# Performance work log

Measured on AMD Instinct MI355X. Metric: run time of the kernel, lower is better.

## Reference

```python
import jax, jax.numpy as jnp
import numpy as np

B, S, H = 8, 512, 768
NH, DH = 12, 64
I = 3072
E = 8
TOPK = 2
EPS = 1e-12


def _ln(x, g, b):
    m = jnp.mean(x, axis=-1, keepdims=True)
    v = jnp.mean(jnp.square(x - m), axis=-1, keepdims=True)
    return (x - m) * jax.lax.rsqrt(v + EPS) * g + b


def setup_inputs() -> dict:
    key = jax.random.key(0)
    ks = jax.random.split(key, 20)
    s_h = 1.0 / np.sqrt(H)
    s_i = 1.0 / np.sqrt(I)
    inp = {
        "hidden_states": jax.random.normal(ks[0], (B, S, H), jnp.float32),
        "Wq": jax.random.normal(ks[1], (H, H), jnp.float32) * s_h,
        "bq": jnp.zeros((H,), jnp.float32),
        "Wk": jax.random.normal(ks[2], (H, H), jnp.float32) * s_h,
        "bk": jnp.zeros((H,), jnp.float32),
        "Wv": jax.random.normal(ks[3], (H, H), jnp.float32) * s_h,
        "bv": jnp.zeros((H,), jnp.float32),
        "Wo": jax.random.normal(ks[4], (H, H), jnp.float32) * s_h,
        "bo": jnp.zeros((H,), jnp.float32),
        "ln_attn_g": jnp.ones((H,), jnp.float32),
        "ln_attn_b": jnp.zeros((H,), jnp.float32),
        "ln_ffn_g": jnp.ones((H,), jnp.float32),
        "ln_ffn_b": jnp.zeros((H,), jnp.float32),
        "Wr": jax.random.normal(ks[5], (H, E), jnp.float32) * s_h,
        "br": jnp.zeros((E,), jnp.float32),
        "W_up": jax.random.normal(ks[6], (E, H, I), jnp.float32) * s_h,
        "b_up": jnp.zeros((E, I), jnp.float32),
        "W_new": jax.random.normal(ks[7], (E, H, I), jnp.float32) * s_h,
        "b_new": jnp.zeros((E, I), jnp.float32),
        "W_down": jax.random.normal(ks[8], (E, I, H), jnp.float32) * s_i,
        "b_down": jnp.zeros((E, H), jnp.float32),
    }
    return inp


def reference(hidden_states, Wq, bq, Wk, bk, Wv, bv, Wo, bo,
              ln_attn_g, ln_attn_b, ln_ffn_g, ln_ffn_b,
              Wr, br, W_up, b_up, W_new, b_new, W_down, b_down):
    x = hidden_states
    # --- BertSelfAttention ---
    q = (x @ Wq + bq).reshape(B, S, NH, DH).transpose(0, 2, 1, 3)
    k = (x @ Wk + bk).reshape(B, S, NH, DH).transpose(0, 2, 1, 3)
    v = (x @ Wv + bv).reshape(B, S, NH, DH).transpose(0, 2, 1, 3)
    scores = jnp.einsum("bhqd,bhkd->bhqk", q, k) / np.sqrt(DH)
    probs = jax.nn.softmax(scores, axis=-1)
    ctx = jnp.einsum("bhqk,bhkd->bhqd", probs, v)
    ctx = ctx.transpose(0, 2, 1, 3).reshape(B, S, H)
    # --- BertSelfOutput: dense + residual + LayerNorm ---
    attention_output = _ln(ctx @ Wo + bo + x, ln_attn_g, ln_attn_b)
    # --- feed_forward_chunk: LayerNorm then token top-k MoE ---
    xl = _ln(attention_output, ln_ffn_g, ln_ffn_b)
    router_logits = xl @ Wr + br                      # [B,S,E]
    router_probs = jax.nn.softmax(router_logits, axis=-1)
    topw, topi = jax.lax.top_k(router_probs, TOPK)    # [B,S,K]
    topw = topw / jnp.sum(topw, axis=-1, keepdims=True)
    gates = jnp.sum(jax.nn.one_hot(topi, E, dtype=xl.dtype) * topw[..., None], axis=-2)  # [B,S,E]
    # --- experts (BertExpert: gelu(up(x)) * new(x) -> down), dense over E ---
    up = jax.nn.gelu(jnp.einsum("bsh,ehi->ebsi", xl, W_up) + b_up[:, None, None, :], approximate=False)
    gate_h = jnp.einsum("bsh,ehi->ebsi", xl, W_new) + b_new[:, None, None, :]
    y = jnp.einsum("ebsi,eih->ebsh", up * gate_h, W_down) + b_down[:, None, None, :]
    moe_out = jnp.einsum("ebsh,bse->bsh", y, gates)
    layer_output = moe_out + attention_output
    return layer_output, router_logits
```

## Files before the change

kernel.cpp:

```cpp
#include <hip/hip_runtime.h>
#include <hip/hip_bf16.h>
#include <cmath>


constexpr int cB = 8, cS = 512, cH = 768, cNH = 12, cDH = 64, cI = 3072, cE = 8;
constexpr int cT = cB * cS;
constexpr size_t TH = (size_t)cT * cH;

typedef __hip_bfloat16 bf16;
typedef __attribute__((ext_vector_type(8))) short s8v;
typedef __attribute__((ext_vector_type(4))) float f4v;

constexpr size_t SZ_WEXP     = (size_t)cE * cI * cH / 2;
constexpr size_t OFF_WUP_T   = 0;
constexpr size_t OFF_WNEW_T  = OFF_WUP_T + SZ_WEXP;
constexpr size_t OFF_WDOWN_T = OFF_WNEW_T + SZ_WEXP;
constexpr size_t OFF_QKV     = OFF_WDOWN_T + SZ_WEXP;
constexpr size_t OFF_CTX     = OFF_QKV + 4 * TH;
constexpr size_t OFF_XLB     = OFF_CTX + TH;
constexpr size_t OFF_WGT     = OFF_XLB + TH / 2;
constexpr size_t OFF_COUNTS  = OFF_WGT + 2 * cT;
constexpr size_t OFF_LISTS   = OFF_COUNTS + 16;

__device__ __forceinline__ void glds16(const void* g, void* l) {
    __builtin_amdgcn_global_load_lds(
        (const __attribute__((address_space(1))) unsigned int*)g,
        (__attribute__((address_space(3))) unsigned int*)l, 16, 0, 0);
}

__global__ void init_counts_kernel(int* __restrict__ counts) {
    if (threadIdx.x < cE) counts[threadIdx.x] = 0;
}

__global__ __launch_bounds__(256) void transpose_bf16_kernel(
    const float* __restrict__ src, bf16* __restrict__ dst, int R, int C) {
    __shared__ float tile[64][65];
    const size_t zb = (size_t)blockIdx.z * R * C;
    const int r0 = blockIdx.y * 64, c0 = blockIdx.x * 64;
    const int t = threadIdx.x;
    const int lr = t >> 4, lc = (t & 15) * 4;
#pragma unroll
    for (int i = 0; i < 4; ++i) {
        float4 v = *(const float4*)(src + zb + (size_t)(r0 + lr + i * 16) * C + c0 + lc);
        tile[lr + i * 16][lc + 0] = v.x; tile[lr + i * 16][lc + 1] = v.y;
        tile[lr + i * 16][lc + 2] = v.z; tile[lr + i * 16][lc + 3] = v.w;
    }
    __syncthreads();
#pragma unroll
    for (int i = 0; i < 4; ++i) {
        int cr = lr + i * 16;
        bf16 o[4];
#pragma unroll
        for (int j = 0; j < 4; ++j) o[j] = (bf16)tile[lc + j][cr];
        *(uint2*)(dst + zb + (size_t)(c0 + cr) * R + r0 + lc) = *(uint2*)o;
    }
}

__device__ __forceinline__ void gemm_body128(
    const float* __restrict__ A, const float* __restrict__ B,
    const float* __restrict__ bias, float* __restrict__ C,
    int N, int K, int m0, int n0, int kbeg, int kend, bool addb) {
    __shared__ float As[16 * 132];
    __shared__ float Bs[16 * 128];
    const int t = threadIdx.x;
    const int tx = t & 15, ty = t >> 4;
    const int ar = t >> 2, ac = (t & 3) * 4;
    const float* gB0 = B + (size_t)(kbeg + (t >> 5)) * N + n0 + (t & 31) * 4;
    float* dB0 = Bs + t * 4;
    const float* gA0 = A + (size_t)(m0 + ar) * K + kbeg + ac;
    const float* gA1 = A + (size_t)(m0 + ar + 64) * K + kbeg + ac;
    float acc[8][8] = {};
    float4 a0 = *(const float4*)gA0;
    float4 a1 = *(const float4*)gA1;
    for (int k0 = kbeg; k0 < kend; k0 += 16) {
        glds16(gB0, dB0);
        glds16(gB0 + (size_t)8 * N, dB0 + 1024);
        As[(ac + 0) * 132 + ar] = a0.x; As[(ac + 1) * 132 + ar] = a0.y;
        As[(ac + 2) * 132 + ar] = a0.z; As[(ac + 3) * 132 + ar] = a0.w;
        As[(ac + 0) * 132 + ar + 64] = a1.x; As[(ac + 1) * 132 + ar + 64] = a1.y;
        As[(ac + 2) * 132 + ar + 64] = a1.z; As[(ac + 3) * 132 + ar + 64] = a1.w;
        __syncthreads();
        if (k0 + 16 < kend) {
            gA0 += 16; gA1 += 16;
            a0 = *(const float4*)gA0;
            a1 = *(const float4*)gA1;
        }
#pragma unroll
        for (int kk = 0; kk < 16; ++kk) {
            float a[8], b[8];
            *(float4*)&a[0] = *(const float4*)&As[kk * 132 + ty * 8];
            *(float4*)&a[4] = *(const float4*)&As[kk * 132 + ty * 8 + 4];
            *(float4*)&b[0] = *(const float4*)&Bs[kk * 128 + tx * 4];
            *(float4*)&b[4] = *(const float4*)&Bs[kk * 128 + tx * 4 + 64];
#pragma unroll
            for (int i = 0; i < 8; ++i)
#pragma unroll
                for (int j = 0; j < 8; ++j) acc[i][j] += a[i] * b[j];
        }
        __syncthreads();
        gB0 += (size_t)16 * N;
    }
#pragma unroll
    for (int i = 0; i < 8; ++i) {
        int m = m0 + ty * 8 + i;
        float4 o0, o1;
        o0.x = acc[i][0]; o0.y = acc[i][1]; o0.z = acc[i][2]; o0.w = acc[i][3];
        o1.x = acc[i][4]; o1.y = acc[i][5]; o1.z = acc[i][6]; o1.w = acc[i][7];
        if (addb) {
            o0.x += bias[n0 + tx * 4 + 0]; o0.y += bias[n0 + tx * 4 + 1];
            o0.z += bias[n0 + tx * 4 + 2]; o0.w += bias[n0 + tx * 4 + 3];
            o1.x += bias[n0 + 64 + tx * 4 + 0]; o1.y += bias[n0 + 64 + tx * 4 + 1];
            o1.z += bias[n0 + 64 + tx * 4 + 2]; o1.w += bias[n0 + 64 + tx * 4 + 3];
        }
        *(float4*)(C + (size_t)m * N + n0 + tx * 4) = o0;
        *(float4*)(C + (size_t)m * N + n0 + 64 + tx * 4) = o1;
    }
}

__global__ __launch_bounds__(256) void gemm_qkv_kernel(
    const float* __restrict__ A,
    const float* __restrict__ Wq, const float* __restrict__ Wk,
    const float* __restrict__ Wv,
    const float* __restrict__ bq, const float* __restrict__ bk,
    const float* __restrict__ bv,
    float* __restrict__ q0, float* __restrict__ k0, float* __restrict__ v0,
    float* __restrict__ q1, float* __restrict__ k1, float* __restrict__ v1) {
    const int f = blockIdx.x + 6 * blockIdx.y + 192 * blockIdx.z;
    const int xcd = f & 7, p = f >> 3;
    const int yl = p & 3;
    const int n  = (p >> 2) % 6;
    const int pz = p / 24;
    const int y  = xcd * 4 + yl;
    const int proj = pz >> 1, ks = pz & 1;
    const float* B = (proj == 0) ? Wq : (proj == 1) ? Wk : Wv;
    const float* bias = (proj == 0) ? bq : (proj == 1) ? bk : bv;
    float* C = (proj == 0) ? (ks ? q1 : q0)
             : (proj == 1) ? (ks ? k1 : k0)
                           : (ks ? v1 : v0);
    gemm_body128(A, B, bias, C, cH, cH, y * 128, n * 128,
                 ks * 384, ks * 384 + 384, ks == 0);
}

__global__ __launch_bounds__(256) void reduce_qkv_kernel(
    float* __restrict__ dst2, const float* __restrict__ src2,
    float* __restrict__ v0, const float* __restrict__ v1) {
    const size_t n2 = 2 * TH / 4, n3 = 3 * TH / 4;
    for (size_t i = (size_t)blockIdx.x * 256 + threadIdx.x; i < n3;
         i += (size_t)gridDim.x * 256) {
        if (i < n2) {
            float4 a = ((const float4*)dst2)[i];
            float4 b = ((const float4*)src2)[i];
            a.x += b.x; a.y += b.y; a.z += b.z; a.w += b.w;
            ((float4*)dst2)[i] = a;
        } else {
            size_t j = i - n2;
            float4 a = ((const float4*)v0)[j];
            float4 b = ((const float4*)v1)[j];
            a.x += b.x; a.y += b.y; a.z += b.z; a.w += b.w;
            ((float4*)v0)[j] = a;
        }
    }
}

__global__ __launch_bounds__(256) void gemm_wo_kernel(
    const float* __restrict__ A, const float* __restrict__ W,
    const float* __restrict__ bias,
    float* __restrict__ p0, float* __restrict__ p1,
    float* __restrict__ p2, float* __restrict__ p3) {
    const int f = blockIdx.x + 6 * blockIdx.y + 192 * blockIdx.z;
    const int xcd = f & 7, p = f >> 3;
    const int yl = p & 3;
    const int n  = (p >> 2) % 6;
    const int ks = p / 24;
    const int y  = xcd * 4 + yl;
    float* C = (ks == 0) ? p0 : (ks == 1) ? p1 : (ks == 2) ? p2 : p3;
    gemm_body128(A, W, bias, C, cH, cH, y * 128, n * 128,
                 ks * 192, ks * 192 + 192, ks == 0);
}

__global__ __launch_bounds__(256) void attn_kernel(
    const float* __restrict__ q, const float* __restrict__ k,
    const float* __restrict__ v, float* __restrict__ ctx) {
    __shared__ float sQ[64][68];
    __shared__ float sKV[64][68];
    __shared__ float sS[64][68];
    __shared__ float sM[64], sL[64], sAl[64];
    const int f = blockIdx.x + 8 * blockIdx.y + 96 * blockIdx.z;
    const int xcd = f & 7, p = f >> 3;
    const int q0 = (p & 7) * 64;
    const int hbg = xcd * 12 + (p >> 3);
    const int h = hbg % 12, b = hbg / 12;
    const int t = threadIdx.x;
    const int lr = t >> 2, lq = (t & 3) * 16;
    {
        const float* gq = q + (size_t)(b * cS + q0 + lr) * cH + h * cDH + lq;
#pragma unroll
        for (int j = 0; j < 4; ++j) {
            float4 x = *(const float4*)(gq + j * 4);
            x.x *= 0.125f; x.y *= 0.125f; x.z *= 0.125f; x.w *= 0.125f;
            *(float4*)&sQ[lr][lq + j * 4] = x;
        }
    }
    if (t < 64) { sM[t] = -1e30f; sL[t] = 0.f; }
    const int c0 = t & 15, rr = (t >> 4) * 4;
    const int d4 = (t & 15) * 4, rp = (t >> 4) * 4;
    const int sr = t >> 2, sc = (t & 3) * 16;
    float4 o_acc[4];
#pragma unroll
    for (int i = 0; i < 4; ++i) o_acc[i] = make_float4(0.f, 0.f, 0.f, 0.f);

    for (int kt = 0; kt < 8; ++kt) {
        float4 kreg[4];
        {
            const float* gk = k + (size_t)(b * cS + kt * 64 + lr) * cH + h * cDH + lq;
#pragma unroll
            for (int j = 0; j < 4; ++j) kreg[j] = *(const float4*)(gk + j * 4);
        }
        __syncthreads();
#pragma unroll
        for (int j = 0; j < 4; ++j) *(float4*)&sKV[lr][lq + j * 4] = kreg[j];
        __syncthreads();
        float accS[4][4] = {};
#pragma unroll
        for (int d = 0; d < 64; d += 4) {
            float4 qv[4], kv[4];
#pragma unroll
            for (int i = 0; i < 4; ++i) qv[i] = *(const float4*)&sQ[rr + i][d];
#pragma unroll
            for (int j = 0; j < 4; ++j) kv[j] = *(const float4*)&sKV[c0 + 16 * j][d];
#pragma unroll
            for (int i = 0; i < 4; ++i)
#pragma unroll
                for (int j = 0; j < 4; ++j)
                    accS[i][j] += qv[i].x * kv[j].x + qv[i].y * kv[j].y +
                                  qv[i].z * kv[j].z + qv[i].w * kv[j].w;
        }
#pragma unroll
        for (int i = 0; i < 4; ++i)
#pragma unroll
            for (int j = 0; j < 4; ++j) sS[rr + i][c0 + 16 * j] = accS[i][j];
        float4 vreg[4];
        {
            const float* gv = v + (size_t)(b * cS + kt * 64 + lr) * cH + h * cDH + lq;
#pragma unroll
            for (int j = 0; j < 4; ++j) vreg[j] = *(const float4*)(gv + j * 4);
        }
        __syncthreads();
        {
            float4 s[4];
#pragma unroll
            for (int j = 0; j < 4; ++j) s[j] = *(const float4*)&sS[sr][sc + j * 4];
            float m = -1e30f;
#pragma unroll
            for (int j = 0; j < 4; ++j)
                m = fmaxf(m, fmaxf(fmaxf(s[j].x, s[j].y), fmaxf(s[j].z, s[j].w)));
            m = fmaxf(m, __shfl_xor(m, 1));
            m = fmaxf(m, __shfl_xor(m, 2));
            float m_old = sM[sr];
            float m_new = fmaxf(m_old, m);
            float sum = 0.f;
#pragma unroll
            for (int j = 0; j < 4; ++j) {
                s[j].x = __expf(s[j].x - m_new); s[j].y = __expf(s[j].y - m_new);
                s[j].z = __expf(s[j].z - m_new); s[j].w = __expf(s[j].w - m_new);
                sum += s[j].x + s[j].y + s[j].z + s[j].w;
                *(float4*)&sS[sr][sc + j * 4] = s[j];
            }
            sum += __shfl_xor(sum, 1);
            sum += __shfl_xor(sum, 2);
            if ((t & 3) == 0) {
                float alpha = __expf(m_old - m_new);
                sAl[sr] = alpha;
                sM[sr] = m_new;
                sL[sr] = sL[sr] * alpha + sum;
            }
        }
#pragma unroll
        for (int j = 0; j < 4; ++j) *(float4*)&sKV[lr][lq + j * 4] = vreg[j];
        __syncthreads();
#pragma unroll
        for (int i = 0; i < 4; ++i) {
            float al = sAl[rp + i];
            o_acc[i].x *= al; o_acc[i].y *= al; o_acc[i].z *= al; o_acc[i].w *= al;
        }
        for (int kk4 = 0; kk4 < 64; kk4 += 4) {
            float4 pv[4], vv[4];
#pragma unroll
            for (int i = 0; i < 4; ++i) pv[i] = *(const float4*)&sS[rp + i][kk4];
#pragma unroll
            for (int j = 0; j < 4; ++j) vv[j] = *(const float4*)&sKV[kk4 + j][d4];
#pragma unroll
            for (int i = 0; i < 4; ++i) {
                o_acc[i].x += pv[i].x * vv[0].x + pv[i].y * vv[1].x +
                              pv[i].z * vv[2].x + pv[i].w * vv[3].x;
                o_acc[i].y += pv[i].x * vv[0].y + pv[i].y * vv[1].y +
                              pv[i].z * vv[2].y + pv[i].w * vv[3].y;
                o_acc[i].z += pv[i].x * vv[0].z + pv[i].y * vv[1].z +
                              pv[i].z * vv[2].z + pv[i].w * vv[3].z;
                o_acc[i].w += pv[i].x * vv[0].w + pv[i].y * vv[1].w +
                              pv[i].z * vv[2].w + pv[i].w * vv[3].w;
            }
        }
    }
    __syncthreads();
#pragma unroll
    for (int i = 0; i < 4; ++i) {
        float inv = 1.0f / sL[rp + i];
        float4 o = o_acc[i];
        o.x *= inv; o.y *= inv; o.z *= inv; o.w *= inv;
        *(float4*)(ctx + (size_t)(b * cS + q0 + rp + i) * cH + h * cDH + d4) = o;
    }
}

__device__ __forceinline__ float block_reduce_sum(float v, float* red) {
#pragma unroll
    for (int o = 32; o; o >>= 1) v += __shfl_xor(v, o);
    __syncthreads();
    if ((threadIdx.x & 63) == 0) red[threadIdx.x >> 6] = v;
    __syncthreads();
    return red[0] + red[1] + red[2] + red[3];
}

__global__ __launch_bounds__(256) void ln_router_kernel(
    const float* __restrict__ dense0, const float* __restrict__ dense1,
    const float* __restrict__ dense2, const float* __restrict__ dense3,
    const float* __restrict__ resid,
    const float* __restrict__ g1, const float* __restrict__ b1,
    const float* __restrict__ g2, const float* __restrict__ b2,
    const float* __restrict__ Wr, const float* __restrict__ br,
    float* __restrict__ out, bf16* __restrict__ xlb,
    float* __restrict__ out_logits, float* __restrict__ wgt,
    int* __restrict__ counts, int* __restrict__ lists) {
    __shared__ float red[4];
    __shared__ float lred[4][8];
    const int t = blockIdx.x, tid = threadIdx.x;
    const size_t base = (size_t)t * cH;
    float v[3], s = 0.f;
#pragma unroll
    for (int i = 0; i < 3; ++i) {
        size_t ix = base + tid + 256 * i;
        v[i] = dense0[ix] + dense1[ix] + dense2[ix] + dense3[ix] + resid[ix];
        s += v[i];
    }
    const float mean = block_reduce_sum(s, red) * (1.0f / cH);
    float vs = 0.f;
#pragma unroll
    for (int i = 0; i < 3; ++i) { float d = v[i] - mean; vs += d * d; }
    const float rstd = rsqrtf(block_reduce_sum(vs, red) * (1.0f / cH) + 1e-12f);
    float a[3], s2 = 0.f;
#pragma unroll
    for (int i = 0; i < 3; ++i) {
        a[i] = (v[i] - mean) * rstd * g1[tid + 256 * i] + b1[tid + 256 * i];
        out[base + tid + 256 * i] = a[i];
        s2 += a[i];
    }
    const float mean2 = block_reduce_sum(s2, red) * (1.0f / cH);
    float vs2 = 0.f;
#pragma unroll
    for (int i = 0; i < 3; ++i) { float d = a[i] - mean2; vs2 += d * d; }
    const float rstd2 = rsqrtf(block_reduce_sum(vs2, red) * (1.0f / cH) + 1e-12f);
    float xl[3];
#pragma unroll
    for (int i = 0; i < 3; ++i) {
        xl[i] = (a[i] - mean2) * rstd2 * g2[tid + 256 * i] + b2[tid + 256 * i];
        xlb[base + tid + 256 * i] = (bf16)xl[i];
    }
    float lg[cE] = {};
#pragma unroll
    for (int i = 0; i < 3; ++i) {
        const float* wr = Wr + (size_t)(tid + 256 * i) * cE;
#pragma unroll
        for (int e = 0; e < cE; ++e) lg[e] += xl[i] * wr[e];
    }
#pragma unroll
    for (int e = 0; e < cE; ++e)
#pragma unroll
        for (int o = 32; o; o >>= 1) lg[e] += __shfl_xor(lg[e], o);
    if ((tid & 63) == 0)
#pragma unroll
        for (int e = 0; e < cE; ++e) lred[tid >> 6][e] = lg[e];
    __syncthreads();
    if (tid == 0) {
        float logits[cE];
#pragma unroll
        for (int e = 0; e < cE; ++e) {
            logits[e] = lred[0][e] + lred[1][e] + lred[2][e] + lred[3][e] + br[e];
            out_logits[(size_t)t * cE + e] = logits[e];
        }
        int i0 = 0;
        for (int e = 1; e < cE; ++e) if (logits[e] > logits[i0]) i0 = e;
        int i1 = (i0 == 0) ? 1 : 0;
        for (int e = 0; e < cE; ++e)
            if (e != i0 && logits[e] > logits[i1]) i1 = e;
        float e1 = __expf(logits[i1] - logits[i0]);
        float w0 = 1.0f / (1.0f + e1);
        float w1 = e1 * w0;
        wgt[t * 2 + 0] = w0;
        wgt[t * 2 + 1] = w1;
        int p0 = atomicAdd(&counts[i0], 1);
        lists[i0 * cT + p0] = t * 2 + 0;
        int p1 = atomicAdd(&counts[i1], 1);
        lists[i1 * cT + p1] = t * 2 + 1;
    }
}

__global__ __launch_bounds__(256) void expert_up_mfma_kernel(
    const bf16* __restrict__ xlb,
    const bf16* __restrict__ WupT, const bf16* __restrict__ WnewT,
    const float* __restrict__ b_up, const float* __restrict__ b_new,
    const int* __restrict__ counts, const int* __restrict__ lists,
    bf16* __restrict__ act) {
    const int e = blockIdx.z;
    const int cnt = counts[e];
    const int m0 = blockIdx.y * 128;
    if (m0 >= cnt) return;
    const int n0 = blockIdx.x * 64;
    __shared__ short sA[128 * 32], sB1[64 * 32], sB2[64 * 32];
    __shared__ int rowa[128];
    const int t = threadIdx.x;
    if (t < 128) {
        int idx = m0 + t;
        rowa[t] = (idx < cnt) ? lists[e * cT + idx] : -1;
    }
    __syncthreads();
    const int lane = t & 63, w = t >> 6;
    const int wm = (w >> 1) * 64, wn = (w & 1) * 32;
    const int rA0 = t >> 2, kc8 = (t & 3) * 8;
    int a0 = rowa[rA0], a1 = rowa[rA0 + 64];
    const bf16* gA0 = xlb + (size_t)(a0 < 0 ? 0 : (a0 >> 1)) * cH + kc8;
    const bf16* gA1 = xlb + (size_t)(a1 < 0 ? 0 : (a1 >> 1)) * cH + kc8;
    const bf16* B1 = WupT + (size_t)e * cI * cH;
    const bf16* B2 = WnewT + (size_t)e * cI * cH;
    const bf16* gB1 = B1 + (size_t)(n0 + rA0) * cH + kc8;
    const bf16* gB2 = B2 + (size_t)(n0 + rA0) * cH + kc8;
    short* dA0 = sA + t * 8;   short* dA1 = sA + (t + 256) * 8;
    short* dB1 = sB1 + t * 8;  short* dB2 = sB2 + t * 8;
    f4v zero = {0.f, 0.f, 0.f, 0.f};
    f4v acc1[4][2], acc2[4][2];
#pragma unroll
    for (int i = 0; i < 4; ++i)
#pragma unroll
        for (int j = 0; j < 2; ++j) { acc1[i][j] = zero; acc2[i][j] = zero; }
    const int fr = lane & 15, kg = (lane >> 4) * 8;
    for (int kk = 0; kk < cH; kk += 32) {
        glds16(gA0, dA0); glds16(gA1, dA1);
        glds16(gB1, dB1); glds16(gB2, dB2);
        __syncthreads();
        s8v af[4], bf1[2], bf2[2];
#pragma unroll
        for (int i = 0; i < 4; ++i)
            af[i] = *(const s8v*)(sA + (wm + i * 16 + fr) * 32 + kg);
#pragma unroll
        for (int j = 0; j < 2; ++j) {
            bf1[j] = *(const s8v*)(sB1 + (wn + j * 16 + fr) * 32 + kg);
            bf2[j] = *(const s8v*)(sB2 + (wn + j * 16 + fr) * 32 + kg);
        }
#pragma unroll
        for (int mi = 0; mi < 4; ++mi)
#pragma unroll
            for (int ni = 0; ni < 2; ++ni) {
                acc1[mi][ni] = __builtin_amdgcn_mfma_f32_16x16x32_bf16(
                    af[mi], bf1[ni], acc1[mi][ni], 0, 0, 0);
                acc2[mi][ni] = __builtin_amdgcn_mfma_f32_16x16x32_bf16(
                    af[mi], bf2[ni], acc2[mi][ni], 0, 0, 0);
            }
        __syncthreads();
        gA0 += 32; gA1 += 32; gB1 += 32; gB2 += 32;
    }
    const int cn = lane & 15, rq = (lane >> 4) * 4;
#pragma unroll
    for (int mi = 0; mi < 4; ++mi)
#pragma unroll
        for (int r = 0; r < 4; ++r) {
            int ml = wm + mi * 16 + rq + r;
            int a = rowa[ml];
            if (a < 0) continue;
            bf16* orow = act + (size_t)a * cI + n0 + wn;
#pragma unroll
            for (int ni = 0; ni < 2; ++ni) {
                int nl = ni * 16 + cn;
                float up = acc1[mi][ni][r] + b_up[e * cI + n0 + wn + nl];
                float nw = acc2[mi][ni][r] + b_new[e * cI + n0 + wn + nl];
                float g = 0.5f * up * (1.0f + erff(up * 0.70710678118654752f));
                orow[nl] = (bf16)(g * nw);
            }
        }
}

__global__ __launch_bounds__(256) void expert_down_mfma_kernel(
    const bf16* __restrict__ act, const bf16* __restrict__ WdownT,
    const float* __restrict__ b_down,
    const int* __restrict__ counts, const int* __restrict__ lists,
    const float* __restrict__ wgt, float* __restrict__ out) {
    const int e = blockIdx.z;
    const int cnt = counts[e];
    const int m0 = blockIdx.y * 128;
    if (m0 >= cnt) return;
    const int n0 = blockIdx.x * 128;
    __shared__ short sA[128 * 32], sB[128 * 32];
    __shared__ int rowa[128];
    const int t = threadIdx.x;
    if (t < 128) {
        int idx = m0 + t;
        rowa[t] = (idx < cnt) ? lists[e * cT + idx] : -1;
    }
    __syncthreads();
    const int lane = t & 63, w = t >> 6;
    const int wm = (w >> 1) * 64, wn = (w & 1) * 64;
    const int rA0 = t >> 2, kc8 = (t & 3) * 8;
    int a0 = rowa[rA0], a1 = rowa[rA0 + 64];
    const bf16* gA0 = act + (size_t)(a0 < 0 ? 0 : a0) * cI + kc8;
    const bf16* gA1 = act + (size_t)(a1 < 0 ? 0 : a1) * cI + kc8;
    const bf16* BT = WdownT + (size_t)e * cH * cI;
    const bf16* gB0 = BT + (size_t)(n0 + rA0) * cI + kc8;
    const bf16* gB1 = BT + (size_t)(n0 + rA0 + 64) * cI + kc8;
    short* dA0 = sA + t * 8;       short* dA1 = sA + (t + 256) * 8;
    short* dB0 = sB + t * 8;       short* dB1 = sB + (t + 256) * 8;
    f4v zero = {0.f, 0.f, 0.f, 0.f};
    f4v acc[4][4];
#pragma unroll
    for (int i = 0; i < 4; ++i)
#pragma unroll
        for (int j = 0; j < 4; ++j) acc[i][j] = zero;
    const int fr = lane & 15, kg = (lane >> 4) * 8;
    for (int kk = 0; kk < cI; kk += 32) {
        glds16(gA0, dA0); glds16(gA1, dA1);
        glds16(gB0, dB0); glds16(gB1, dB1);
        __syncthreads();
        s8v af[4], bf[4];
#pragma unroll
        for (int i = 0; i < 4; ++i) af[i] = *(const s8v*)(sA + (wm + i * 16 + fr) * 32 + kg);
#pragma unroll
        for (int i = 0; i < 4; ++i) bf[i] = *(const s8v*)(sB + (wn + i * 16 + fr) * 32 + kg);
#pragma unroll
        for (int mi = 0; mi < 4; ++mi)
#pragma unroll
            for (int ni = 0; ni < 4; ++ni)
                acc[mi][ni] = __builtin_amdgcn_mfma_f32_16x16x32_bf16(
                    af[mi], bf[ni], acc[mi][ni], 0, 0, 0);
        __syncthreads();
        gA0 += 32; gA1 += 32; gB0 += 32; gB1 += 32;
    }
    const int cn = lane & 15, rq = (lane >> 4) * 4;
#pragma unroll
    for (int mi = 0; mi < 4; ++mi)
#pragma unroll
        for (int r = 0; r < 4; ++r) {
            int ml = wm + mi * 16 + rq + r;
            int a = rowa[ml];
            if (a < 0) continue;
            int token = a >> 1;
            float wv = wgt[a];
#pragma unroll
            for (int ni = 0; ni < 4; ++ni) {
                int n = n0 + wn + ni * 16 + cn;
                atomicAdd(&out[(size_t)token * cH + n],
                          wv * (acc[mi][ni][r] + b_down[e * cH + n]));
            }
        }
}

extern "C" void kernel_launch(void* const* d_in, const int* in_sizes, int n_in,
                              void* d_out, int out_size, void* d_ws, size_t ws_size,
                              hipStream_t stream) {
    const float* x      = (const float*)d_in[0];
    const float* Wq     = (const float*)d_in[1];
    const float* bq     = (const float*)d_in[2];
    const float* Wk     = (const float*)d_in[3];
    const float* bk     = (const float*)d_in[4];
    const float* Wv     = (const float*)d_in[5];
    const float* bv     = (const float*)d_in[6];
    const float* Wo     = (const float*)d_in[7];
    const float* bo     = (const float*)d_in[8];
    const float* ln1g   = (const float*)d_in[9];
    const float* ln1b   = (const float*)d_in[10];
    const float* ln2g   = (const float*)d_in[11];
    const float* ln2b   = (const float*)d_in[12];
    const float* Wr     = (const float*)d_in[13];
    const float* br     = (const float*)d_in[14];
    const float* W_up   = (const float*)d_in[15];
    const float* b_up   = (const float*)d_in[16];
    const float* W_new  = (const float*)d_in[17];
    const float* b_new  = (const float*)d_in[18];
    const float* W_down = (const float*)d_in[19];
    const float* b_down = (const float*)d_in[20];

    float* out = (float*)d_out;
    float* ws  = (float*)d_ws;

    bf16* WupT   = (bf16*)(ws + OFF_WUP_T);
    bf16* WnewT  = (bf16*)(ws + OFF_WNEW_T);
    bf16* WdownT = (bf16*)(ws + OFF_WDOWN_T);
    float* q     = ws + OFF_QKV;
    float* k     = ws + OFF_QKV + TH;
    float* v     = ws + OFF_QKV + 2 * TH;
    float* tmp   = ws + OFF_QKV + 3 * TH;
    bf16* act    = (bf16*)(ws + OFF_QKV);
    float* ctx   = ws + OFF_CTX;
    bf16* xlb    = (bf16*)(ws + OFF_XLB);
    float* wgt   = ws + OFF_WGT;
    int* counts  = (int*)(ws + OFF_COUNTS);
    int* lists   = (int*)(ws + OFF_LISTS);

    init_counts_kernel<<<1, 64, 0, stream>>>(counts);

    transpose_bf16_kernel<<<dim3(48, 12, cE), 256, 0, stream>>>(W_up, WupT, cH, cI);
    transpose_bf16_kernel<<<dim3(48, 12, cE), 256, 0, stream>>>(W_new, WnewT, cH, cI);
    transpose_bf16_kernel<<<dim3(12, 48, cE), 256, 0, stream>>>(W_down, WdownT, cI, cH);

    gemm_qkv_kernel<<<dim3(cH / 128, cT / 128, 6), 256, 0, stream>>>(
        x, Wq, Wk, Wv, bq, bk, bv, q, k, v, tmp, ctx, out);
    reduce_qkv_kernel<<<2048, 256, 0, stream>>>(q, tmp, v, out);
    attn_kernel<<<dim3(cS / 64, cNH, cB), 256, 0, stream>>>(q, k, v, ctx);
    gemm_wo_kernel<<<dim3(cH / 128, cT / 128, 4), 256, 0, stream>>>(
        ctx, Wo, bo, q, k, v, tmp);
    ln_router_kernel<<<cT, 256, 0, stream>>>(
        q, k, v, tmp, x, ln1g, ln1b, ln2g, ln2b, Wr, br,
        out, xlb, out + TH, wgt, counts, lists);

    expert_up_mfma_kernel<<<dim3(cI / 64, cT / 128, cE), 256, 0, stream>>>(
        xlb, WupT, WnewT, b_up, b_new, counts, lists, act);
    expert_down_mfma_kernel<<<dim3(cH / 128, cT / 128, cE), 256, 0, stream>>>(
        act, WdownT, b_down, counts, lists, wgt, out);
}
```

Baseline: 1.056 ms.

## Remap expert GEMM blocks so each XCD reuses one weight column tile

The expert up and down kernels now compute a linear block id and remap it so that all M-blocks sharing one (expert, N-tile) weight slice land on the same XCD, since consecutive blocks are dispatched round-robin across the eight XCDs. This is meant to improve L2 reuse of the bf16 weight tiles. The fp32 GEMM body also drops its register prefetch of the next A tile and loads A at the top of each iteration, which shortens register live ranges but exposes global load latency before the barrier. The remap relies on the grid dimensions matching the hardcoded constants.

```diff
diff --git a/kernel.cpp b/kernel.cpp
--- a/kernel.cpp
+++ b/kernel.cpp
@@ -67,12 +67,10 @@
     const int ar = t >> 2, ac = (t & 3) * 4;
     const float* gB0 = B + (size_t)(kbeg + (t >> 5)) * N + n0 + (t & 31) * 4;
     float* dB0 = Bs + t * 4;
-    const float* gA0 = A + (size_t)(m0 + ar) * K + kbeg + ac;
-    const float* gA1 = A + (size_t)(m0 + ar + 64) * K + kbeg + ac;
     float acc[8][8] = {};
-    float4 a0 = *(const float4*)gA0;
-    float4 a1 = *(const float4*)gA1;
     for (int k0 = kbeg; k0 < kend; k0 += 16) {
+        float4 a0 = *(const float4*)(A + (size_t)(m0 + ar) * K + k0 + ac);
+        float4 a1 = *(const float4*)(A + (size_t)(m0 + ar + 64) * K + k0 + ac);
         glds16(gB0, dB0);
         glds16(gB0 + (size_t)8 * N, dB0 + 1024);
         As[(ac + 0) * 132 + ar] = a0.x; As[(ac + 1) * 132 + ar] = a0.y;
@@ -80,11 +78,6 @@
         As[(ac + 0) * 132 + ar + 64] = a1.x; As[(ac + 1) * 132 + ar + 64] = a1.y;
         As[(ac + 2) * 132 + ar + 64] = a1.z; As[(ac + 3) * 132 + ar + 64] = a1.w;
         __syncthreads();
-        if (k0 + 16 < kend) {
-            gA0 += 16; gA1 += 16;
-            a0 = *(const float4*)gA0;
-            a1 = *(const float4*)gA1;
-        }
 #pragma unroll
         for (int kk = 0; kk < 16; ++kk) {
             float a[8], b[8];
@@ -410,11 +403,17 @@
     const float* __restrict__ b_up, const float* __restrict__ b_new,
     const int* __restrict__ counts, const int* __restrict__ lists,
     bf16* __restrict__ act) {
-    const int e = blockIdx.z;
+    const int hh = blockIdx.x + 48 * blockIdx.y + 1536 * blockIdx.z;
+    const int xcd = hh & 7;
+    const int r = hh >> 3;
+    const int mb = r & 31;
+    const int cq = r >> 5;
+    const int c = cq * 8 + xcd;
+    const int e = c / 48, n0b = c % 48;
     const int cnt = counts[e];
-    const int m0 = blockIdx.y * 128;
+    const int m0 = mb * 128;
     if (m0 >= cnt) return;
-    const int n0 = blockIdx.x * 64;
+    const int n0 = n0b * 64;
     __shared__ short sA[128 * 32], sB1[64 * 32], sB2[64 * 32];
     __shared__ int rowa[128];
     const int t = threadIdx.x;
@@ -471,16 +470,16 @@
 #pragma unroll
     for (int mi = 0; mi < 4; ++mi)
 #pragma unroll
-        for (int r = 0; r < 4; ++r) {
-            int ml = wm + mi * 16 + rq + r;
+        for (int r2 = 0; r2 < 4; ++r2) {
+            int ml = wm + mi * 16 + rq + r2;
             int a = rowa[ml];
             if (a < 0) continue;
             bf16* orow = act + (size_t)a * cI + n0 + wn;
 #pragma unroll
             for (int ni = 0; ni < 2; ++ni) {
                 int nl = ni * 16 + cn;
-                float up = acc1[mi][ni][r] + b_up[e * cI + n0 + wn + nl];
-                float nw = acc2[mi][ni][r] + b_new[e * cI + n0 + wn + nl];
+                float up = acc1[mi][ni][r2] + b_up[e * cI + n0 + wn + nl];
+                float nw = acc2[mi][ni][r2] + b_new[e * cI + n0 + wn + nl];
                 float g = 0.5f * up * (1.0f + erff(up * 0.70710678118654752f));
                 orow[nl] = (bf16)(g * nw);
             }
@@ -492,11 +491,17 @@
     const float* __restrict__ b_down,
     const int* __restrict__ counts, const int* __restrict__ lists,
     const float* __restrict__ wgt, float* __restrict__ out) {
-    const int e = blockIdx.z;
+    const int hh = blockIdx.x + 6 * blockIdx.y + 192 * blockIdx.z;
+    const int xcd = hh & 7;
+    const int r = hh >> 3;
+    const int mb = r & 31;
+    const int cq = r >> 5;
+    const int c = cq * 8 + xcd;
+    const int e = c / 6, n0b = c % 6;
     const int cnt = counts[e];
-    const int m0 = blockIdx.y * 128;
+    const int m0 = mb * 128;
     if (m0 >= cnt) return;
-    const int n0 = blockIdx.x * 128;
+    const int n0 = n0b * 128;
     __shared__ short sA[128 * 32], sB[128 * 32];
     __shared__ int rowa[128];
     const int t = threadIdx.x;
@@ -545,8 +550,8 @@
 #pragma unroll
     for (int mi = 0; mi < 4; ++mi)
 #pragma unroll
-        for (int r = 0; r < 4; ++r) {
-            int ml = wm + mi * 16 + rq + r;
+        for (int r2 = 0; r2 < 4; ++r2) {
+            int ml = wm + mi * 16 + rq + r2;
             int a = rowa[ml];
             if (a < 0) continue;
             int token = a >> 1;
@@ -555,7 +560,7 @@
             for (int ni = 0; ni < 4; ++ni) {
                 int n = n0 + wn + ni * 16 + cn;
                 atomicAdd(&out[(size_t)token * cH + n],
-                          wv * (acc[mi][ni][r] + b_down[e * cH + n]));
+                          wv * (acc[mi][ni][r2] + b_down[e * cH + n]));
             }
         }
 }
```

New measurement: 1.063 ms. No clear change (+0.7%).
